# Performance work log

Hardware: AMD Instinct MI355X
Metric: run time of the kernel (lower is better)

Reference implementation:

```python
import jax, jax.numpy as jnp
import numpy as np

N, A, G, C = 16, 4096, 256, 80
ALPHA, GAMMA, CLS_LAMBDA = 0.25, 2.0, 1.0
BIG = 1e8


def setup_inputs() -> dict:
    key = jax.random.key(0)
    k1, k2, k3, k4, k5, k6 = jax.random.split(key, 6)
    return {
        "gt_padded": jax.random.uniform(k1, (N, G, 4), dtype=jnp.float32),
        "prop_boxes": jax.random.uniform(k2, (N, A, 4), dtype=jnp.float32),
        "pred_boxes": jax.random.uniform(k3, (N, A, 4), dtype=jnp.float32),
        "class_logits": jax.random.normal(k4, (N, A, C), dtype=jnp.float32),
        "gt_masks": jax.random.randint(k5, (N, G), 0, 2).astype(bool),
        "gt_classes": jax.random.randint(k6, (N, G), 0, C),
    }


def _box_distances(b1, b2):
    # b1: [N, A, 4], b2: [N, G, 4] -> pairwise L1 distance [N, A, G]
    return jnp.abs(b1[:, :, None, :] - b2[:, None, :, :]).sum(-1)


def _sigmoid_focal_loss(logits, one_hot, alpha, gamma):
    p = jax.nn.sigmoid(logits)
    # stable BCE-with-logits
    ce = jnp.maximum(logits, 0.0) - logits * one_hot + jnp.log1p(jnp.exp(-jnp.abs(logits)))
    p_t = p * one_hot + (1.0 - p) * (1.0 - one_hot)
    loss = ce * (1.0 - p_t) ** gamma
    alpha_t = alpha * one_hot + (1.0 - alpha) * (1.0 - one_hot)
    return alpha_t * loss


def reference(gt_padded, prop_boxes, pred_boxes, class_logits, gt_masks, gt_classes):
    mask_row = gt_masks[:, None, :]  # [N, 1, G]

    # proposal -> gt pairwise L1, masked argmin over gt axis
    prop_d = jnp.where(mask_row, _box_distances(prop_boxes, gt_padded), BIG)
    closest = jnp.argmin(prop_d, axis=-1)  # [N, A]

    # projection loss: pred -> gt distance gathered at proposals' closest gt
    pred_d = jnp.where(mask_row, _box_distances(pred_boxes, gt_padded), BIG)
    proj = jnp.take_along_axis(pred_d, closest[..., None], axis=2)[..., 0]  # [N, A]
    mask_gathered = jnp.take_along_axis(gt_masks, closest, axis=1)  # [N, A]
    projection_loss = jnp.where(mask_gathered, proj, 0.0)

    # classification target: class of closest gt (0 when image has no gt)
    nonempty = gt_masks.any(-1)  # [N]
    target = jnp.take_along_axis(gt_classes, closest, axis=1)  # [N, A]
    target = jnp.where(nonempty[:, None], target, 0)

    one_hot = jax.nn.one_hot(target, C, dtype=class_logits.dtype)
    cls = _sigmoid_focal_loss(class_logits, one_hot, ALPHA, GAMMA).mean(-1)  # [N, A]
    classification_loss = jnp.where(nonempty[:, None], cls, 0.0) * CLS_LAMBDA

    return classification_loss, projection_loss
```

## Files before the change

### kernel.cpp

```cpp
#include <hip/hip_runtime.h>

#define N_ 16
#define A_ 4096
#define G_ 256
#define C_ 80
#define ALPHA_ 0.25f
#define BIG_ 1e8f


__global__ __launch_bounds__(256) void cbppl_fused_kernel(
    const float* __restrict__ gt_padded,
    const float* __restrict__ prop_boxes,
    const float* __restrict__ pred_boxes,
    const float* __restrict__ class_logits,
    const int*   __restrict__ gt_masks,
    const int*   __restrict__ gt_classes,
    float* __restrict__ out_cls,
    float* __restrict__ out_proj)
{
    __shared__ float4 s_gt[G_];
    __shared__ int    s_cls[G_];

    const int t   = threadIdx.x;
    const int n   = blockIdx.x >> 7;
    const int a   = ((blockIdx.x & 127) << 5) + (t >> 3);
    const int sub = t & 7;

    {
        const int gi = n * G_ + t;
        float4 g4 = ((const float4*)gt_padded)[gi];
        if (!gt_masks[gi]) { g4.x = BIG_; g4.y = BIG_; g4.z = BIG_; g4.w = BIG_; }
        s_gt[t]  = g4;
        s_cls[t] = gt_classes[gi];
    }
    __syncthreads();

    const float4 pb = ((const float4*)prop_boxes)[n * A_ + a];

    float mind    = INFINITY;
    int   closest = 0;
    #pragma unroll 8
    for (int g = sub; g < G_; g += 8) {
        const float4 gb = s_gt[g];
        const float d = fabsf(pb.x - gb.x) + fabsf(pb.y - gb.y)
                      + fabsf(pb.z - gb.z) + fabsf(pb.w - gb.w);
        if (d < mind) { mind = d; closest = g; }
    }
    #pragma unroll
    for (int off = 1; off < 8; off <<= 1) {
        const float od = __shfl_xor(mind, off, 64);
        const int   oc = __shfl_xor(closest, off, 64);
        if (od < mind || (od == mind && oc < closest)) { mind = od; closest = oc; }
    }
    const int nonempty = (mind < BIG_);

    const float4 qb = ((const float4*)pred_boxes)[n * A_ + a];
    const float4 cb = s_gt[closest];
    const float  pd = fabsf(qb.x - cb.x) + fabsf(qb.y - cb.y)
                    + fabsf(qb.z - cb.z) + fabsf(qb.w - cb.w);
    const float proj = nonempty ? pd : 0.0f;

    const int target = nonempty ? s_cls[closest] : 0;

    const float2* lg2 = (const float2*)(class_logits + ((size_t)(n * A_ + a)) * C_);
    float acc = 0.0f;
    #pragma unroll
    for (int j = 0; j < 5; ++j) {
        const float2 x2 = lg2[sub + j * 8];
        const float xs[2] = {x2.x, x2.y};
        #pragma unroll
        for (int k = 0; k < 2; ++k) {
            const int   c  = (sub + j * 8) * 2 + k;
            const float x  = xs[k];
            const float oh = (c == target) ? 1.0f : 0.0f;
            const float ax = fabsf(x);
            const float e  = __expf(-ax);
            const float ce = fmaxf(x, 0.0f) - x * oh + __logf(1.0f + e);
            const float r  = __builtin_amdgcn_rcpf(1.0f + e);
            const float p  = (x >= 0.0f) ? r : e * r;
            const float pt = oh ? p : (1.0f - p);
            const float om = 1.0f - pt;
            const float at = oh ? ALPHA_ : (1.0f - ALPHA_);
            acc += at * (ce * om * om);
        }
    }
    acc += __shfl_xor(acc, 1, 64);
    acc += __shfl_xor(acc, 2, 64);
    acc += __shfl_xor(acc, 4, 64);

    if (sub == 0) {
        const int oidx = n * A_ + a;
        out_cls[oidx]  = nonempty ? acc * (1.0f / (float)C_) : 0.0f;
        out_proj[oidx] = proj;
    }
}

extern "C" void kernel_launch(void* const* d_in, const int* in_sizes, int n_in,
                              void* d_out, int out_size, void* d_ws, size_t ws_size,
                              hipStream_t stream) {
    const float* gt_padded    = (const float*)d_in[0];
    const float* prop_boxes   = (const float*)d_in[1];
    const float* pred_boxes   = (const float*)d_in[2];
    const float* class_logits = (const float*)d_in[3];
    const int*   gt_masks     = (const int*)d_in[4];
    const int*   gt_classes   = (const int*)d_in[5];

    float* out = (float*)d_out;
    float* out_cls  = out;
    float* out_proj = out + N_ * A_;

    dim3 grid(N_ * A_ / 32);
    dim3 block(256);
    cbppl_fused_kernel<<<grid, block, 0, stream>>>(
        gt_padded, prop_boxes, pred_boxes, class_logits,
        gt_masks, gt_classes, out_cls, out_proj);
}
```

Baseline: 15.20 us.

## Cache gt boxes in registers and process four anchors per thread group

Each block now handles 64 anchors with 16-lane groups, and each lane keeps 16 gt boxes in registers that are reused across four anchors, instead of re-reading shared memory for every anchor. The argmin is split into a min reduction followed by a reduction over candidate indices. The focal loss is computed as the non-target formula for all classes plus a single target correction, which removes the per-element one-hot selects. Launch bounds now request 4 blocks per CU, and logits are loaded as scalars with stride 16. The risks are higher register pressure and a dependent gather of the target logit.

Measured after the change: 15.31 us. About the same (+0.7%).

```diff
diff --git a/kernel.cpp b/kernel.cpp
--- a/kernel.cpp
+++ b/kernel.cpp
@@ -4,11 +4,11 @@
 #define A_ 4096
 #define G_ 256
 #define C_ 80
-#define ALPHA_ 0.25f
 #define BIG_ 1e8f
+#define LN2_ 0.69314718055994531f
 
 
-__global__ __launch_bounds__(256) void cbppl_fused_kernel(
+__global__ __launch_bounds__(256, 4) void cbppl_fused_kernel(
     const float* __restrict__ gt_padded,
     const float* __restrict__ prop_boxes,
     const float* __restrict__ pred_boxes,
@@ -22,76 +22,91 @@
     __shared__ int    s_cls[G_];
 
     const int t   = threadIdx.x;
-    const int n   = blockIdx.x >> 7;
-    const int a   = ((blockIdx.x & 127) << 5) + (t >> 3);
-    const int sub = t & 7;
+    const int sub = t & 15;
+    const int n   = blockIdx.x >> 6;
+    const int ab  = (blockIdx.x & 63) << 6;
 
     {
-        const int gi = n * G_ + t;
-        float4 g4 = ((const float4*)gt_padded)[gi];
-        if (!gt_masks[gi]) { g4.x = BIG_; g4.y = BIG_; g4.z = BIG_; g4.w = BIG_; }
+        const int gidx = n * G_ + t;
+        float4 g4 = ((const float4*)gt_padded)[gidx];
+        if (!gt_masks[gidx]) { g4.x = BIG_; g4.y = BIG_; g4.z = BIG_; g4.w = BIG_; }
         s_gt[t]  = g4;
-        s_cls[t] = gt_classes[gi];
+        s_cls[t] = gt_classes[gidx];
     }
     __syncthreads();
 
-    const float4 pb = ((const float4*)prop_boxes)[n * A_ + a];
+    float4 b[16];
+    #pragma unroll
+    for (int m = 0; m < 16; ++m) b[m] = s_gt[sub + (m << 4)];
 
-    float mind    = INFINITY;
-    int   closest = 0;
-    #pragma unroll 8
-    for (int g = sub; g < G_; g += 8) {
-        const float4 gb = s_gt[g];
-        const float d = fabsf(pb.x - gb.x) + fabsf(pb.y - gb.y)
-                      + fabsf(pb.z - gb.z) + fabsf(pb.w - gb.w);
-        if (d < mind) { mind = d; closest = g; }
-    }
-    #pragma unroll
-    for (int off = 1; off < 8; off <<= 1) {
-        const float od = __shfl_xor(mind, off, 64);
-        const int   oc = __shfl_xor(closest, off, 64);
-        if (od < mind || (od == mind && oc < closest)) { mind = od; closest = oc; }
-    }
-    const int nonempty = (mind < BIG_);
+    for (int p = 0; p < 4; ++p) {
+        const int ai  = ((t >> 6) << 4) + (p << 2) + ((t >> 4) & 3);
+        const int row = n * A_ + ab + ai;
 
-    const float4 qb = ((const float4*)pred_boxes)[n * A_ + a];
-    const float4 cb = s_gt[closest];
-    const float  pd = fabsf(qb.x - cb.x) + fabsf(qb.y - cb.y)
-                    + fabsf(qb.z - cb.z) + fabsf(qb.w - cb.w);
-    const float proj = nonempty ? pd : 0.0f;
+        const float4 pb = ((const float4*)prop_boxes)[row];
+        const float4 qb = ((const float4*)pred_boxes)[row];
 
-    const int target = nonempty ? s_cls[closest] : 0;
+        const float* lrow = class_logits + (size_t)row * C_;
+        float xv[5];
+        #pragma unroll
+        for (int k = 0; k < 5; ++k) xv[k] = lrow[sub + (k << 4)];
 
-    const float2* lg2 = (const float2*)(class_logits + ((size_t)(n * A_ + a)) * C_);
-    float acc = 0.0f;
-    #pragma unroll
-    for (int j = 0; j < 5; ++j) {
-        const float2 x2 = lg2[sub + j * 8];
-        const float xs[2] = {x2.x, x2.y};
+        float dloc = INFINITY;
+        int   mloc = 0;
         #pragma unroll
-        for (int k = 0; k < 2; ++k) {
-            const int   c  = (sub + j * 8) * 2 + k;
-            const float x  = xs[k];
-            const float oh = (c == target) ? 1.0f : 0.0f;
-            const float ax = fabsf(x);
-            const float e  = __expf(-ax);
-            const float ce = fmaxf(x, 0.0f) - x * oh + __logf(1.0f + e);
-            const float r  = __builtin_amdgcn_rcpf(1.0f + e);
-            const float p  = (x >= 0.0f) ? r : e * r;
-            const float pt = oh ? p : (1.0f - p);
-            const float om = 1.0f - pt;
-            const float at = oh ? ALPHA_ : (1.0f - ALPHA_);
-            acc += at * (ce * om * om);
+        for (int m = 0; m < 16; ++m) {
+            const float d = fabsf(pb.x - b[m].x) + fabsf(pb.y - b[m].y)
+                          + fabsf(pb.z - b[m].z) + fabsf(pb.w - b[m].w);
+            if (d < dloc) { dloc = d; mloc = m; }
         }
-    }
-    acc += __shfl_xor(acc, 1, 64);
-    acc += __shfl_xor(acc, 2, 64);
-    acc += __shfl_xor(acc, 4, 64);
+        const int iloc = (mloc << 4) + sub;
 
-    if (sub == 0) {
-        const int oidx = n * A_ + a;
-        out_cls[oidx]  = nonempty ? acc * (1.0f / (float)C_) : 0.0f;
-        out_proj[oidx] = proj;
+        float dmin = dloc;
+        #pragma unroll
+        for (int k = 1; k < 16; k <<= 1) dmin = fminf(dmin, __shfl_xor(dmin, k, 64));
+        int cand = (dloc == dmin) ? iloc : 0x7FFFFFFF;
+        #pragma unroll
+        for (int k = 1; k < 16; k <<= 1) cand = min(cand, __shfl_xor(cand, k, 64));
+        const int closest  = cand;
+        const int nonempty = (dmin < BIG_);
+
+        const float4 cb     = s_gt[closest];
+        const int    target = s_cls[closest];
+        const float  pd = fabsf(qb.x - cb.x) + fabsf(qb.y - cb.y)
+                        + fabsf(qb.z - cb.z) + fabsf(qb.w - cb.w);
+
+        float acc = 0.0f;
+        #pragma unroll
+        for (int k = 0; k < 5; ++k) {
+            const float x  = xv[k];
+            const float e  = __expf(-fabsf(x));
+            const float tt = 1.0f + e;
+            const float sp = fmaf(LN2_, __log2f(tt), fmaxf(x, 0.0f));
+            const float r  = __builtin_amdgcn_rcpf(tt);
+            const float pp = (x >= 0.0f) ? r : e * r;
+            acc += sp * pp * pp;
+        }
+        acc *= 0.75f;
+
+        {
+            const float xt = lrow[target];
+            const float e  = __expf(-fabsf(xt));
+            const float tt = 1.0f + e;
+            const float sp = fmaf(LN2_, __log2f(tt), fmaxf(xt, 0.0f));
+            const float r  = __builtin_amdgcn_rcpf(tt);
+            const float pp = (xt >= 0.0f) ? r : e * r;
+            const float q  = 1.0f - pp;
+            const float corr = 0.25f * (sp - xt) * q * q - 0.75f * sp * pp * pp;
+            if ((target & 15) == sub) acc += corr;
+        }
+
+        #pragma unroll
+        for (int k = 1; k < 16; k <<= 1) acc += __shfl_xor(acc, k, 64);
+
+        if (sub == 0) {
+            out_cls[row]  = nonempty ? acc * (1.0f / (float)C_) : 0.0f;
+            out_proj[row] = nonempty ? pd : 0.0f;
+        }
     }
 }
 
@@ -109,7 +124,7 @@
     float* out_cls  = out;
     float* out_proj = out + N_ * A_;
 
-    dim3 grid(N_ * A_ / 32);
+    dim3 grid(N_ * A_ / 64);
     dim3 block(256);
     cbppl_fused_kernel<<<grid, block, 0, stream>>>(
         gt_padded, prop_boxes, pred_boxes, class_logits,
```
